# Optimization experiments

Hardware: AMD Instinct MI355X
Metric: run time of the kernel (lower is better)

The kernel has to match this reference:

```python
import jax, jax.numpy as jnp
import numpy as np

NUM_HEADS = 16
HEAD_DIM = 64  # hidden_size // num_heads = 1024 // 16


def setup_inputs() -> dict:
    key = jax.random.key(0)
    ks = jax.random.split(key, 5)
    B, S, D = 4, 2048, 1024
    scale = 1.0 / np.sqrt(D)
    return {
        "hidden_states": jax.random.normal(ks[0], (B, S, D), dtype=jnp.float32),
        "Wq": jax.random.normal(ks[1], (D, D), dtype=jnp.float32) * scale,
        "Wk": jax.random.normal(ks[2], (D, D), dtype=jnp.float32) * scale,
        "Wv": jax.random.normal(ks[3], (D, D), dtype=jnp.float32) * scale,
        "Wo": jax.random.normal(ks[4], (D, D), dtype=jnp.float32) * scale,
    }


def reference(hidden_states, Wq, Wk, Wv, Wo):
    B, S, D = hidden_states.shape
    H, hd = NUM_HEADS, HEAD_DIM
    # torch nn.Linear(y = x @ W.T), bias=False
    q = (hidden_states @ Wq.T).reshape(B, S, H, hd)
    k = (hidden_states @ Wk.T).reshape(B, S, H, hd)
    v = (hidden_states @ Wv.T).reshape(B, S, H, hd)
    q = q / jnp.sqrt(jnp.float32(hd))
    # scores: [B, H, S, S] — module materializes full score matrix
    scores = jnp.einsum("bqhd,bkhd->bhqk", q, k)
    weights = jax.nn.softmax(scores, axis=-1)
    attn = jnp.einsum("bhqk,bkhd->bqhd", weights, v).reshape(B, S, D)
    return attn @ Wo.T
```

## Files before the change

kernel.cpp:

```cpp
#include <hip/hip_runtime.h>

using u16 = unsigned short;
using u32 = unsigned int;
typedef __attribute__((ext_vector_type(8))) short bf16x8;
typedef __attribute__((ext_vector_type(4))) short bf16x4;
typedef __attribute__((ext_vector_type(4))) float f32x4;
typedef __attribute__((ext_vector_type(16))) float f32x16;
typedef __attribute__((ext_vector_type(4))) u32 u32x4;

__device__ __forceinline__ u16 f2bf(float f) {
  u32 u = __builtin_bit_cast(u32, f);
  u += 0x7FFFu + ((u >> 16) & 1u);
  return (u16)(u >> 16);
}

__device__ __forceinline__ void load_lds16(const void* g, void* l) {
  typedef const __attribute__((address_space(1))) u32 GA;
  typedef __attribute__((address_space(3))) u32 LA;
  __builtin_amdgcn_global_load_lds((GA*)g, (LA*)l, 16, 0, 0);
}

__device__ __forceinline__ bf16x4 tr16(const u16* p) {
  typedef __attribute__((address_space(3))) const u16 LT;
  bf16x4 d;
  asm volatile("ds_read_b64_tr_b16 %0, %1" : "=v"(d) : "v"((LT*)p));
  return d;
}

__device__ __forceinline__ float exp2_fast(float x) {
  float r;
  asm("v_exp_f32 %0, %1" : "=v"(r) : "v"(x));
  return r;
}

__device__ __forceinline__ u32 cvt_pk_bf16(float lo, float hi) {
  u32 r;
  asm("v_cvt_pk_bf16_f32 %0, %1, %2" : "=v"(r) : "v"(lo), "v"(hi));
  return r;
}

__device__ __forceinline__ void permlane32_swap(u32& a, u32& b) {
  asm volatile("v_permlane32_swap_b32 %0, %1" : "+v"(a), "+v"(b));
}

__global__ void cvt_bf16(const float* __restrict__ src, u16* __restrict__ dst,
                         int n4, float scale) {
  int i = blockIdx.x * blockDim.x + threadIdx.x;
  if (i >= n4) return;
  float4 v = reinterpret_cast<const float4*>(src)[i];
  ushort4 o;
  o.x = f2bf(v.x * scale);
  o.y = f2bf(v.y * scale);
  o.z = f2bf(v.z * scale);
  o.w = f2bf(v.w * scale);
  reinterpret_cast<ushort4*>(dst)[i] = o;
}

__global__ void cvt_w4(const float* __restrict__ Wq, const float* __restrict__ Wk,
                       const float* __restrict__ Wv, const float* __restrict__ Wo,
                       u16* __restrict__ dst, int n4seg, float qscale) {
  int i = blockIdx.x * blockDim.x + threadIdx.x;
  int seg = i / n4seg, off = i - seg * n4seg;
  const float* src = seg == 0 ? Wq : seg == 1 ? Wk : seg == 2 ? Wv : Wo;
  float sc = seg == 0 ? qscale : 1.0f;
  float4 v = reinterpret_cast<const float4*>(src)[off];
  ushort4 o;
  o.x = f2bf(v.x * sc);
  o.y = f2bf(v.y * sc);
  o.z = f2bf(v.z * sc);
  o.w = f2bf(v.w * sc);
  reinterpret_cast<ushort4*>(dst)[i] = o;
}

template <typename OutT>
__global__ __launch_bounds__(256, 2) void gemm_bt(
    const u16* __restrict__ A, const u16* __restrict__ Bw,
    OutT* __restrict__ C, int M, int N, int K) {
  __shared__ u16 At[128 * 32];
  __shared__ u16 Bt[128 * 32];
  const int tid = threadIdx.x;
  const int wid = tid >> 6, lane = tid & 63;
  const int wr = wid >> 1, wc = wid & 1;
  const int laneR = lane & 15, laneG = lane >> 4;
  const int laneK = laneG * 8;

  const int nbm = M >> 7;
  const int cpx = gridDim.x >> 3;
  const int id = blockIdx.x;
  const int swz = (id & 7) * cpx + (id >> 3);
  const int bm = swz % nbm, bn = swz / nbm;

  f32x4 acc[4][4];
#pragma unroll
  for (int i = 0; i < 4; ++i)
#pragma unroll
    for (int j = 0; j < 4; ++j) acc[i][j] = f32x4{0.f, 0.f, 0.f, 0.f};

  const int e0 = tid * 8;
  const int r0 = e0 >> 5, c0 = e0 & 31;
  const u16* Ab = A + (size_t)(bm * 128) * K;
  const u16* Bb = Bw + (size_t)(bn * 128) * K;

  for (int k0 = 0; k0 < K; k0 += 32) {
#pragma unroll
    for (int i = 0; i < 2; ++i) {
      load_lds16(Ab + (size_t)(i * 64 + r0) * K + k0 + c0, &At[(i * 256 + wid * 64) * 8]);
      load_lds16(Bb + (size_t)(i * 64 + r0) * K + k0 + c0, &Bt[(i * 256 + wid * 64) * 8]);
    }
    __syncthreads();
    bf16x8 af[4], bfr[4];
#pragma unroll
    for (int i = 0; i < 4; ++i)
      af[i] = *(const bf16x8*)&At[(wr * 64 + i * 16 + laneR) * 32 + laneK];
#pragma unroll
    for (int j = 0; j < 4; ++j)
      bfr[j] = *(const bf16x8*)&Bt[(wc * 64 + j * 16 + laneR) * 32 + laneK];
#pragma unroll
    for (int i = 0; i < 4; ++i)
#pragma unroll
      for (int j = 0; j < 4; ++j)
        acc[i][j] = __builtin_amdgcn_mfma_f32_16x16x32_bf16(af[i], bfr[j], acc[i][j], 0, 0, 0);
    __syncthreads();
  }

  const int crow = bm * 128 + wr * 64;
  const int ccol = bn * 128 + wc * 64;
#pragma unroll
  for (int i = 0; i < 4; ++i)
#pragma unroll
    for (int j = 0; j < 4; ++j)
#pragma unroll
      for (int r = 0; r < 4; ++r) {
        int row = crow + i * 16 + laneG * 4 + r;
        int col = ccol + j * 16 + laneR;
        float v = acc[i][j][r];
        if constexpr (sizeof(OutT) == 2)
          C[(size_t)row * N + col] = f2bf(v);
        else
          C[(size_t)row * N + col] = v;
      }
}

template <int MH, int NH>
__device__ __forceinline__ void mfma_quad(f32x4 (&acc)[8][4], bf16x8 (&afr)[4][2],
                                          bf16x8 (&bfr)[2][2]) {
  __builtin_amdgcn_s_setprio(1);
#pragma unroll
  for (int m = 0; m < 4; ++m)
#pragma unroll
    for (int n = 0; n < 2; ++n)
#pragma unroll
      for (int ks = 0; ks < 2; ++ks)
        acc[MH * 4 + m][NH * 2 + n] = __builtin_amdgcn_mfma_f32_16x16x32_bf16(
            afr[m][ks], bfr[n][ks], acc[MH * 4 + m][NH * 2 + n], 0, 0, 0);
  __builtin_amdgcn_s_setprio(0);
}

#define GBAR() __builtin_amdgcn_s_barrier()
#define WAITL()                                            \
  do {                                                     \
    asm volatile("s_waitcnt lgkmcnt(0)" ::: "memory");     \
    __builtin_amdgcn_sched_barrier(0);                     \
  } while (0)
#define WAITLV()                                                    \
  do {                                                              \
    asm volatile("s_waitcnt vmcnt(2) lgkmcnt(0)" ::: "memory");     \
    __builtin_amdgcn_sched_barrier(0);                              \
  } while (0)

template <typename OutT>
__global__ __launch_bounds__(512, 2) void gemm256(
    const u16* __restrict__ A, const u16* __restrict__ Bw,
    OutT* __restrict__ C, int M, int N, int K) {
  __shared__ __align__(16) char ldsb[131072];
  const int tid = threadIdx.x;
  const int wid = tid >> 6, lane = tid & 63;
  const int wr = wid >> 2, wc = wid & 3;
  const int laneR = lane & 15, laneG = lane >> 4;
  const int swzR = (laneR & 7) << 4;

  const int nbm = M >> 8;
  const int cpx = gridDim.x >> 3;
  const int id = blockIdx.x;
  const int swzid = (id & 7) * cpx + (id >> 3);
  const int bm = swzid % nbm, bn = swzid / nbm;

  const u16* Ab = A + (size_t)(bm * 256) * K;
  const u16* Bb = Bw + (size_t)(bn * 256) * K;

  const int s_r = tid >> 3;
  const int s_k = ((tid & 7) ^ (s_r & 7)) * 8;

  auto stage_half = [&](const u16* Xb, int regio, int buf, int hh, int kt) {
    char* d = ldsb + regio + buf * 32768 + hh * 16384 + wid * 1024;
#pragma unroll
    for (int j = 0; j < 2; ++j)
      load_lds16(Xb + (size_t)(hh * 128 + j * 64 + s_r) * K + kt * 64 + s_k,
                 d + j * 8192);
  };
  auto rdA = [&](int buf, int mh, int m, int ks) -> bf16x8 {
    return *(const bf16x8*)(ldsb + buf * 32768 + wr * 16384 +
                            (mh * 64 + m * 16 + laneR) * 128 +
                            ((ks * 64 + laneG * 16) ^ swzR));
  };
  auto rdB = [&](int buf, int nh, int n, int ks) -> bf16x8 {
    return *(const bf16x8*)(ldsb + 65536 + buf * 32768 + (wc >> 1) * 16384 +
                            ((wc & 1) * 64 + nh * 32 + n * 16 + laneR) * 128 +
                            ((ks * 64 + laneG * 16) ^ swzR));
  };

  f32x4 acc[8][4];
#pragma unroll
  for (int i = 0; i < 8; ++i)
#pragma unroll
    for (int j = 0; j < 4; ++j) acc[i][j] = f32x4{0.f, 0.f, 0.f, 0.f};

  bf16x8 afr[4][2], bfr[2][2];
  auto readAB = [&](int buf, int mh, int nh) {
#pragma unroll
    for (int m = 0; m < 4; ++m) {
      afr[m][0] = rdA(buf, mh, m, 0);
      afr[m][1] = rdA(buf, mh, m, 1);
    }
#pragma unroll
    for (int n = 0; n < 2; ++n) {
      bfr[n][0] = rdB(buf, nh, n, 0);
      bfr[n][1] = rdB(buf, nh, n, 1);
    }
  };
  auto readB = [&](int buf, int nh) {
#pragma unroll
    for (int n = 0; n < 2; ++n) {
      bfr[n][0] = rdB(buf, nh, n, 0);
      bfr[n][1] = rdB(buf, nh, n, 1);
    }
  };

  const int NT = K >> 6, NI = K >> 7;

  stage_half(Ab, 0, 0, 0, 0);
  stage_half(Ab, 0, 0, 1, 0);
  stage_half(Bb, 65536, 0, 0, 0);
  stage_half(Bb, 65536, 0, 1, 0);
  stage_half(Ab, 0, 1, 0, 1);
  asm volatile("s_waitcnt vmcnt(2)" ::: "memory");
  GBAR();

  for (int i = 0; i < NI; ++i) {
    const int t1 = (2 * i + 1) & (NT - 1);
    const int t2 = (2 * i + 2) & (NT - 1);
    const int t3 = (2 * i + 3) & (NT - 1);
    readAB(0, 0, 0); stage_half(Ab, 0, 1, 1, t1); WAITL(); GBAR();
    mfma_quad<0, 0>(acc, afr, bfr); GBAR();
    readB(0, 1); stage_half(Bb, 65536, 1, 0, t1); WAITL(); GBAR();
    mfma_quad<0, 1>(acc, afr, bfr); GBAR();
    readAB(0, 1, 0); stage_half(Bb, 65536, 1, 1, t1); WAITL(); GBAR();
    mfma_quad<1, 0>(acc, afr, bfr); GBAR();
    readB(0, 1); stage_half(Ab, 0, 0, 0, t2); WAITLV(); GBAR();
    mfma_quad<1, 1>(acc, afr, bfr); GBAR();
    readAB(1, 0, 0); stage_half(Ab, 0, 0, 1, t2); WAITL(); GBAR();
    mfma_quad<0, 0>(acc, afr, bfr); GBAR();
    readB(1, 1); stage_half(Bb, 65536, 0, 0, t2); WAITL(); GBAR();
    mfma_quad<0, 1>(acc, afr, bfr); GBAR();
    readAB(1, 1, 0); stage_half(Bb, 65536, 0, 1, t2); WAITL(); GBAR();
    mfma_quad<1, 0>(acc, afr, bfr); GBAR();
    readB(1, 1); stage_half(Ab, 0, 1, 0, t3); WAITLV(); GBAR();
    mfma_quad<1, 1>(acc, afr, bfr); GBAR();
  }

  const int crow = bm * 256 + wr * 128;
  const int ccol = bn * 256 + wc * 64;
#pragma unroll
  for (int mf = 0; mf < 8; ++mf)
#pragma unroll
    for (int nf = 0; nf < 4; ++nf)
#pragma unroll
      for (int r = 0; r < 4; ++r) {
        int row = crow + mf * 16 + laneG * 4 + r;
        int col = ccol + nf * 16 + laneR;
        float v = acc[mf][nf][r];
        if constexpr (sizeof(OutT) == 2)
          C[(size_t)row * N + col] = f2bf(v);
        else
          C[(size_t)row * N + col] = v;
      }
}

__global__ __launch_bounds__(256, 4) void flash_attn(
    const u16* __restrict__ QKV, u16* __restrict__ O) {
  constexpr int S = 2048, DQ = 3072, DO = 1024;
  __shared__ u16 Kt[2][4096];
  __shared__ u16 Vt[2][4096];
  const int tid = threadIdx.x, wid = tid >> 6, lane = tid & 63;
  const int lq = lane & 31, hi = lane >> 5;
  const int qt = blockIdx.x;
  const int b = blockIdx.y >> 4, h = blockIdx.y & 15;

  const size_t bq = (size_t)b * S * DQ;
  const u16* Qg = QKV + bq + h * 64;
  const u16* Kg = QKV + bq + 1024 + h * 64;
  const u16* Vg = QKV + bq + 2048 + h * 64;
  const int qrow0 = qt * 128 + wid * 32;

  const int k_kv = tid >> 3;
  const int k_col = ((tid & 7) ^ (k_kv & 7)) * 8;
  const int v_kv = ((tid >> 5) << 2) | ((tid >> 1) & 3);
  const int v_hd = (((tid >> 3) & 3) << 4) | ((tid & 1) << 3);

  bf16x8 qf[4];
#pragma unroll
  for (int kc = 0; kc < 4; ++kc)
    qf[kc] = *(const bf16x8*)&Qg[(size_t)(qrow0 + lq) * DQ + kc * 16 + hi * 8];

  f32x16 o0, o1;
#pragma unroll
  for (int r = 0; r < 16; ++r) { o0[r] = 0.f; o1[r] = 0.f; }
  float l = 0.f;

  auto stage = [&](int buf, int kv0) {
#pragma unroll
    for (int ch = 0; ch < 2; ++ch) {
      load_lds16(Kg + (size_t)(kv0 + ch * 32 + k_kv) * DQ + k_col,
                 &Kt[buf][ch * 2048 + wid * 512]);
      load_lds16(Vg + (size_t)(kv0 + ch * 32 + v_kv) * DQ + v_hd,
                 &Vt[buf][ch * 2048 + wid * 512]);
    }
  };

  stage(0, 0);
  __syncthreads();

  for (int t = 0; t < 32; ++t) {
    const int cur = t & 1;
    stage(cur ^ 1, ((t + 1) & 31) * 64);

    f32x16 st[2];
#pragma unroll
    for (int blk = 0; blk < 2; ++blk) {
#pragma unroll
      for (int r = 0; r < 16; ++r) st[blk][r] = 0.f;
      bf16x8 kf[4];
#pragma unroll
      for (int kc = 0; kc < 4; ++kc) {
        int kv = blk * 32 + lq;
        int byt = kv * 128 + ((kc * 32 + hi * 16) ^ ((kv & 7) << 4));
        kf[kc] = *(const bf16x8*)((const char*)&Kt[cur][0] + byt);
      }
      __builtin_amdgcn_s_setprio(1);
#pragma unroll
      for (int kc = 0; kc < 4; ++kc)
        st[blk] = __builtin_amdgcn_mfma_f32_32x32x16_bf16(kf[kc], qf[kc], st[blk], 0, 0, 0);
      __builtin_amdgcn_s_setprio(0);
    }

    float ps = 0.f;
#pragma unroll
    for (int blk = 0; blk < 2; ++blk)
#pragma unroll
      for (int r = 0; r < 16; ++r) {
        float p = exp2_fast(st[blk][r]);
        st[blk][r] = p;
        ps += p;
      }
    l += ps;

    u32 W0[8], W1[8];
#pragma unroll
    for (int r2 = 0; r2 < 8; ++r2) {
      W0[r2] = cvt_pk_bf16(st[0][2 * r2], st[0][2 * r2 + 1]);
      W1[r2] = cvt_pk_bf16(st[1][2 * r2], st[1][2 * r2 + 1]);
    }
    bf16x8 pb[4];
#pragma unroll
    for (int ks = 0; ks < 2; ++ks) {
      u32 a0 = W0[4 * ks], a2 = W0[4 * ks + 2];
      u32 a1 = W0[4 * ks + 1], a3 = W0[4 * ks + 3];
      permlane32_swap(a0, a2);
      permlane32_swap(a1, a3);
      pb[ks] = __builtin_bit_cast(bf16x8, u32x4{a0, a1, a2, a3});
    }
#pragma unroll
    for (int ks = 0; ks < 2; ++ks) {
      u32 a0 = W1[4 * ks], a2 = W1[4 * ks + 2];
      u32 a1 = W1[4 * ks + 1], a3 = W1[4 * ks + 3];
      permlane32_swap(a0, a2);
      permlane32_swap(a1, a3);
      pb[2 + ks] = __builtin_bit_cast(bf16x8, u32x4{a0, a1, a2, a3});
    }

#pragma unroll
    for (int c2 = 0; c2 < 2; ++c2) {
      bf16x4 vh[4][2];
      const int hb = c2 * 2 + ((lane >> 4) & 1);
#pragma unroll
      for (int ks = 0; ks < 4; ++ks)
#pragma unroll
        for (int p2 = 0; p2 < 2; ++p2) {
          int a = ks * 4 + hi * 2 + p2;
          vh[ks][p2] = tr16(&Vt[cur][(a * 4 + hb) * 64 + (lane & 15) * 4]);
        }
      asm volatile("s_waitcnt lgkmcnt(0)" ::: "memory");
      __builtin_amdgcn_sched_barrier(0);
      __builtin_amdgcn_s_setprio(1);
      f32x16 oc = c2 ? o1 : o0;
#pragma unroll
      for (int ks = 0; ks < 4; ++ks) {
        bf16x8 vf = __builtin_shufflevector(vh[ks][0], vh[ks][1], 0, 1, 2, 3, 4, 5, 6, 7);
        oc = __builtin_amdgcn_mfma_f32_32x32x16_bf16(vf, pb[ks], oc, 0, 0, 0);
      }
      if (c2) o1 = oc; else o0 = oc;
      __builtin_amdgcn_s_setprio(0);
    }

    __syncthreads();
  }

  l += __shfl_xor(l, 32);
  const float inv = 1.0f / l;
  const size_t boo = (size_t)b * S * DO + h * 64;
  const size_t qb = boo + (size_t)(qrow0 + lq) * DO;
#pragma unroll
  for (int r = 0; r < 16; ++r) {
    int hd = (r & 3) + 8 * (r >> 2) + 4 * hi;
    O[qb + hd] = f2bf(o0[r] * inv);
    O[qb + 32 + hd] = f2bf(o1[r] * inv);
  }
}

extern "C" void kernel_launch(void* const* d_in, const int* in_sizes, int n_in,
                              void* d_out, int out_size, void* d_ws, size_t ws_size,
                              hipStream_t stream) {
  const float* hs = (const float*)d_in[0];
  const float* Wq = (const float*)d_in[1];
  const float* Wk = (const float*)d_in[2];
  const float* Wv = (const float*)d_in[3];
  const float* Wo = (const float*)d_in[4];
  float* out = (float*)d_out;

  constexpr int Bn = 4, S = 2048, Dm = 1024;
  constexpr int M = Bn * S;
  constexpr size_t SZ = (size_t)M * Dm;
  constexpr size_t WSZ = (size_t)Dm * Dm;

  u16* wsp = (u16*)d_ws;
  u16* QKVb = wsp;
  u16* hs16 = QKVb + (size_t)M * 3072;
  u16* Ob = hs16;
  u16* W16 = hs16 + SZ;
  u16* Wo16 = W16 + 3 * WSZ;
  (void)ws_size; (void)in_sizes; (void)n_in; (void)out_size;

  cvt_bf16<<<(int)(SZ / 4 / 256), 256, 0, stream>>>(hs, hs16, (int)(SZ / 4), 1.0f);
  cvt_w4<<<(int)(4 * WSZ / 4 / 256), 256, 0, stream>>>(
      Wq, Wk, Wv, Wo, W16, (int)(WSZ / 4), 0.125f * 1.44269504f);

  gemm256<u16><<<(M / 256) * (3072 / 256), 512, 0, stream>>>(hs16, W16, QKVb, M, 3072, Dm);

  flash_attn<<<dim3(S / 128, Bn * 16), 256, 0, stream>>>(QKVb, Ob);

  gemm_bt<float><<<(M / 128) * (Dm / 128), 256, 0, stream>>>(Ob, Wo16, out, M, Dm, Dm);
}
```

Measured before the change: 205.2 us.

## Double flash-attention block to 512 threads and reorder GEMM barriers

Flash attention now runs 512-thread blocks that each cover 256 query rows, so every K/V tile staged into LDS is shared by twice as many waves and each thread issues one load per tile instead of two. Separately, the GEMM wait macros now put the workgroup barrier before the LDS/VMEM waitcnt and drop the sched_barrier, which lets the compiler schedule more freely around those points. Risks: fewer blocks in the attention grid, higher LDS pressure per CU, and possible ordering hazards once the sched_barrier is gone.

```diff
diff --git a/kernel.cpp b/kernel.cpp
--- a/kernel.cpp
+++ b/kernel.cpp
@@ -157,15 +157,15 @@
 }
 
 #define GBAR() __builtin_amdgcn_s_barrier()
-#define WAITL()                                            \
+#define PWAIT()                                            \
   do {                                                     \
+    GBAR();                                                \
     asm volatile("s_waitcnt lgkmcnt(0)" ::: "memory");     \
-    __builtin_amdgcn_sched_barrier(0);                     \
   } while (0)
-#define WAITLV()                                                    \
+#define PWAITV()                                                    \
   do {                                                              \
+    GBAR();                                                         \
     asm volatile("s_waitcnt vmcnt(2) lgkmcnt(0)" ::: "memory");     \
-    __builtin_amdgcn_sched_barrier(0);                              \
   } while (0)
 
 template <typename OutT>
@@ -250,21 +250,21 @@
     const int t1 = (2 * i + 1) & (NT - 1);
     const int t2 = (2 * i + 2) & (NT - 1);
     const int t3 = (2 * i + 3) & (NT - 1);
-    readAB(0, 0, 0); stage_half(Ab, 0, 1, 1, t1); WAITL(); GBAR();
+    readAB(0, 0, 0); stage_half(Ab, 0, 1, 1, t1); PWAIT();
     mfma_quad<0, 0>(acc, afr, bfr); GBAR();
-    readB(0, 1); stage_half(Bb, 65536, 1, 0, t1); WAITL(); GBAR();
+    readB(0, 1); stage_half(Bb, 65536, 1, 0, t1); PWAIT();
     mfma_quad<0, 1>(acc, afr, bfr); GBAR();
-    readAB(0, 1, 0); stage_half(Bb, 65536, 1, 1, t1); WAITL(); GBAR();
+    readAB(0, 1, 0); stage_half(Bb, 65536, 1, 1, t1); PWAIT();
     mfma_quad<1, 0>(acc, afr, bfr); GBAR();
-    readB(0, 1); stage_half(Ab, 0, 0, 0, t2); WAITLV(); GBAR();
+    readB(0, 1); stage_half(Ab, 0, 0, 0, t2); PWAITV();
     mfma_quad<1, 1>(acc, afr, bfr); GBAR();
-    readAB(1, 0, 0); stage_half(Ab, 0, 0, 1, t2); WAITL(); GBAR();
+    readAB(1, 0, 0); stage_half(Ab, 0, 0, 1, t2); PWAIT();
     mfma_quad<0, 0>(acc, afr, bfr); GBAR();
-    readB(1, 1); stage_half(Bb, 65536, 0, 0, t2); WAITL(); GBAR();
+    readB(1, 1); stage_half(Bb, 65536, 0, 0, t2); PWAIT();
     mfma_quad<0, 1>(acc, afr, bfr); GBAR();
-    readAB(1, 1, 0); stage_half(Bb, 65536, 0, 1, t2); WAITL(); GBAR();
+    readAB(1, 1, 0); stage_half(Bb, 65536, 0, 1, t2); PWAIT();
     mfma_quad<1, 0>(acc, afr, bfr); GBAR();
-    readB(1, 1); stage_half(Ab, 0, 1, 0, t3); WAITLV(); GBAR();
+    readB(1, 1); stage_half(Ab, 0, 1, 0, t3); PWAITV();
     mfma_quad<1, 1>(acc, afr, bfr); GBAR();
   }
 
@@ -286,7 +286,7 @@
       }
 }
 
-__global__ __launch_bounds__(256, 4) void flash_attn(
+__global__ __launch_bounds__(512, 4) void flash_attn(
     const u16* __restrict__ QKV, u16* __restrict__ O) {
   constexpr int S = 2048, DQ = 3072, DO = 1024;
   __shared__ u16 Kt[2][4096];
@@ -300,7 +300,7 @@
   const u16* Qg = QKV + bq + h * 64;
   const u16* Kg = QKV + bq + 1024 + h * 64;
   const u16* Vg = QKV + bq + 2048 + h * 64;
-  const int qrow0 = qt * 128 + wid * 32;
+  const int qrow0 = qt * 256 + wid * 32;
 
   const int k_kv = tid >> 3;
   const int k_col = ((tid & 7) ^ (k_kv & 7)) * 8;
@@ -318,13 +318,8 @@
   float l = 0.f;
 
   auto stage = [&](int buf, int kv0) {
-#pragma unroll
-    for (int ch = 0; ch < 2; ++ch) {
-      load_lds16(Kg + (size_t)(kv0 + ch * 32 + k_kv) * DQ + k_col,
-                 &Kt[buf][ch * 2048 + wid * 512]);
-      load_lds16(Vg + (size_t)(kv0 + ch * 32 + v_kv) * DQ + v_hd,
-                 &Vt[buf][ch * 2048 + wid * 512]);
-    }
+    load_lds16(Kg + (size_t)(kv0 + k_kv) * DQ + k_col, &Kt[buf][wid * 512]);
+    load_lds16(Vg + (size_t)(kv0 + v_kv) * DQ + v_hd, &Vt[buf][wid * 512]);
   };
 
   stage(0, 0);
@@ -456,7 +451,7 @@
 
   gemm256<u16><<<(M / 256) * (3072 / 256), 512, 0, stream>>>(hs16, W16, QKVb, M, 3072, Dm);
 
-  flash_attn<<<dim3(S / 128, Bn * 16), 256, 0, stream>>>(QKVb, Ob);
+  flash_attn<<<dim3(S / 256, Bn * 16), 512, 0, stream>>>(QKVb, Ob);
 
   gemm_bt<float><<<(M / 128) * (Dm / 128), 256, 0, stream>>>(Ob, Wo16, out, M, Dm, Dm);
 }
```

Result: faster. 196.9 us (-4.0%).
